# Performance work log

Hardware: AMD Instinct MI355X
Metric: run time of the kernel (lower is better)

## Reference

```python
import jax, jax.numpy as jnp
import numpy as np

B, T, DD, NS, V, E, H, L = 8192, 200, 8, 4, 1000, 32, 256, 2


def setup_inputs() -> dict:
    key = jax.random.key(0)
    ks = jax.random.split(key, 10)
    s = 0.05
    dense = jax.random.normal(ks[0], (B, T, DD), jnp.float32)
    sparse = jax.random.randint(ks[1], (B, T, NS), 0, V)
    lengths = jax.random.randint(ks[2], (B,), 1, T + 1)
    emb_tables = jax.random.normal(ks[3], (NS, V, E), jnp.float32) * s
    Wl = jax.random.normal(ks[4], (H, DD + NS * E), jnp.float32) * s
    bl = jnp.zeros((H,), jnp.float32)
    # axis1: 0 = rnn_entry_exit (even t), 1 = rnn_exit_entry (odd t)
    Wih = jax.random.normal(ks[5], (L, 2, H, H), jnp.float32) * s
    Whh = jax.random.normal(ks[6], (L, 2, H, H), jnp.float32) * s
    bih = jnp.zeros((L, 2, H), jnp.float32)
    bhh = jnp.zeros((L, 2, H), jnp.float32)
    Wout = jax.random.normal(ks[7], (1, H), jnp.float32) * s
    bout = jnp.zeros((1,), jnp.float32)
    return dict(dense=dense, sparse=sparse, lengths=lengths, emb_tables=emb_tables,
                Wl=Wl, bl=bl, Wih=Wih, Whh=Whh, bih=bih, bhh=bhh, Wout=Wout, bout=bout)


def reference(dense, sparse, lengths, emb_tables, Wl, bl, Wih, Whh, bih, bhh, Wout, bout):
    # Padded+mask formulation; equivalent to the packed-sequence loop:
    # finished sequences' hidden states are frozen (== being sliced away),
    # and the final frozen h of the top layer is the per-sequence output.
    # Dropout is identity (eval mode); it is never applied in forward anyway.
    mask = jnp.arange(T)[None, :] < lengths[:, None]        # [B, T]
    d_t = jnp.swapaxes(dense, 0, 1)                          # [T, B, DD]
    s_t = jnp.swapaxes(sparse, 0, 1)                         # [T, B, NS]
    m_t = mask.T                                             # [T, B]

    def embed(st):  # [B, NS] -> [B, NS*E], matching torch.cat of per-feature embeddings
        e = jax.vmap(lambda tab, idx: tab[idx], in_axes=(0, 1), out_axes=1)(emb_tables, st)
        return e.reshape(st.shape[0], NS * E)

    def step(h, xs):  # h: [L, B, H]
        t, dt, st, mt = xs
        x = jnp.concatenate([dt, embed(st)], axis=-1)        # [B, DD+NS*E]
        x = jax.nn.relu(x @ Wl.T + bl)                       # [B, H]
        p = t % 2                                            # which cell set this step
        hs = []
        for i in range(L):
            hn = jnp.tanh(x @ Wih[i, p].T + bih[i, p] + h[i] @ Whh[i, p].T + bhh[i, p])
            hi = jnp.where(mt[:, None], hn, h[i])
            hs.append(hi)
            x = hi
        return jnp.stack(hs), None

    h0 = jnp.zeros((L, B, H), dense.dtype)
    hT, _ = jax.lax.scan(step, h0, (jnp.arange(T), d_t, s_t, m_t))
    return jax.nn.sigmoid(hT[-1] @ Wout.T + bout)[:, 0]     # [B]
```

## Files before the change

### kernel.cpp

```cpp
#include <hip/hip_runtime.h>
#include <math.h>


typedef __attribute__((ext_vector_type(8))) short bf16x8;
typedef __attribute__((ext_vector_type(4))) short s16x4;
typedef __attribute__((ext_vector_type(4))) float f32x4;

#define MFMA(a, b, c) __builtin_amdgcn_mfma_f32_16x16x32_bf16((a), (b), (c), 0, 0, 0)

#define T_  200

#define WLP_OFF   0
#define WIHP_OFF  40960
#define WHHP_OFF  (40960 + 262144)
#define BSUM_BYTE_OFF ((40960 + 262144 + 262144) * 2)

#define XCS 168
#define HS  264
#define SM_XCAT 0
#define SM_XPJ  5376
#define SM_H0   (SM_XPJ + 8448)
#define SM_H1A  (SM_H0 + 8448)
#define SM_H1B  (SM_H1A + 8448)
#define SM_BIAS (SM_H1B + 8448)
#define SM_TOT  (SM_BIAS + 2560)

__device__ __forceinline__ short f2bf(float f) {
    unsigned u = __float_as_uint(f);
    u += 0x7fffu + ((u >> 16) & 1u);
    return (short)(u >> 16);
}
__device__ __forceinline__ float bf2f(short s) {
    return __uint_as_float(((unsigned)(unsigned short)s) << 16);
}
__device__ __forceinline__ float tanh_fast(float x) {
    float e = exp2f(x * 2.88539008f);
    return 1.0f - 2.0f * __builtin_amdgcn_rcpf(e + 1.0f);
}

__global__ void prep_kernel(const float* __restrict__ Wl,
                            const float* __restrict__ Wih,
                            const float* __restrict__ Whh,
                            const float* __restrict__ bih,
                            const float* __restrict__ bhh,
                            short* __restrict__ wsS,
                            float* __restrict__ bsum) {
    int tid = blockIdx.x * 256 + threadIdx.x;
    if (tid < 5120) {
        int mt = tid / 320, rem = tid % 320;
        int kk = rem / 64, lane = rem % 64;
        int o = mt * 16 + (lane & 15);
        int kb = kk * 32 + (lane >> 4) * 8;
        short* dst = wsS + WLP_OFF + tid * 8;
#pragma unroll
        for (int e = 0; e < 8; e++) {
            int k = kb + e;
            dst[e] = f2bf((k < 136) ? Wl[o * 136 + k] : 0.0f);
        }
    } else if (tid < 5120 + 32768) {
        int jj = tid - 5120;
        int mat = jj / 8192, rem = jj % 8192;
        int lane = rem & 63, kk = (rem >> 6) & 7, mt = rem >> 9;
        int o = mt * 16 + (lane & 15);
        int kb = kk * 32 + (lane >> 4) * 8;
        const float* src = Wih + (mat * 256 + o) * 256;
        short* dst = wsS + WIHP_OFF + mat * 65536 + rem * 8;
#pragma unroll
        for (int e = 0; e < 8; e++) dst[e] = f2bf(src[kb + e]);
    } else if (tid < 5120 + 65536) {
        int jj = tid - 37888;
        int mat = jj / 8192, rem = jj % 8192;
        int lane = rem & 63, kk = (rem >> 6) & 7, mt = rem >> 9;
        int o = mt * 16 + (lane & 15);
        int kb = kk * 32 + (lane >> 4) * 8;
        const float* src = Whh + (mat * 256 + o) * 256;
        short* dst = wsS + WHHP_OFF + mat * 65536 + rem * 8;
#pragma unroll
        for (int e = 0; e < 8; e++) dst[e] = f2bf(src[kb + e]);
    } else if (tid < 5120 + 65536 + 1024) {
        int j = tid - 70656;
        bsum[j] = bih[j] + bhh[j];
    }
}

struct GReg { f32x4 e0, e1, dv; };

__device__ __forceinline__ void gather_load(GReg& g, const float* __restrict__ dense,
                                            const int* __restrict__ sparse,
                                            const float* __restrict__ emb,
                                            int b0, int tt, int tid) {
    int gs = tid >> 4, gf = (tid >> 2) & 3, gq = tid & 3;
    int ix = sparse[(b0 + gs) * (T_ * 4) + tt * 4 + gf];
    const float* ep = emb + gf * 32000 + ix * 32 + gq * 8;
    g.e0 = *(const f32x4*)ep;
    g.e1 = *(const f32x4*)(ep + 4);
    if (tid < 64)
        g.dv = *(const f32x4*)(dense + (b0 + (tid >> 1)) * (T_ * 8) + tt * 8 + (tid & 1) * 4);
}
__device__ __forceinline__ void gather_commit(const GReg& g, short* __restrict__ buf, int tid) {
    int gs = tid >> 4, gf = (tid >> 2) & 3, gq = tid & 3;
    s16x4 w0, w1;
#pragma unroll
    for (int r = 0; r < 4; r++) { w0[r] = f2bf(g.e0[r]); w1[r] = f2bf(g.e1[r]); }
    int off = gs * XCS + 8 + gf * 32 + gq * 8;
    *(s16x4*)(buf + off) = w0;
    *(s16x4*)(buf + off + 4) = w1;
    if (tid < 64) {
        s16x4 wd;
#pragma unroll
        for (int r = 0; r < 4; r++) wd[r] = f2bf(g.dv[r]);
        *(s16x4*)(buf + (tid >> 1) * XCS + (tid & 1) * 4) = wd;
    }
}

__device__ __forceinline__ void phaseA(const short* __restrict__ xcat,
                                       short* __restrict__ xpj,
                                       const short* __restrict__ wsS,
                                       const float* __restrict__ blS,
                                       int lane, int lrow, int lgrp, int wid) {
    bf16x8 wl[2][5];
#pragma unroll
    for (int kk = 0; kk < 5; kk++)
#pragma unroll
        for (int mt = 0; mt < 2; mt++)
            wl[mt][kk] = *(const bf16x8*)(wsS + WLP_OFF + (((wid * 2 + mt) * 5 + kk) * 64 + lane) * 8);
    f32x4 xacc[2][2];
#pragma unroll
    for (int mt = 0; mt < 2; mt++) {
        f32x4 bi = *(const f32x4*)(blS + wid * 32 + mt * 16 + lgrp * 4);
        xacc[mt][0] = bi; xacc[mt][1] = bi;
    }
#pragma unroll
    for (int kk = 0; kk < 5; kk++) {
        bf16x8 bxf[2];
#pragma unroll
        for (int nt = 0; nt < 2; nt++)
            bxf[nt] = *(const bf16x8*)(xcat + (nt * 16 + lrow) * XCS + kk * 32 + lgrp * 8);
#pragma unroll
        for (int mt = 0; mt < 2; mt++)
#pragma unroll
            for (int nt = 0; nt < 2; nt++) xacc[mt][nt] = MFMA(wl[mt][kk], bxf[nt], xacc[mt][nt]);
    }
#pragma unroll
    for (int mt = 0; mt < 2; mt++) {
        int o0 = wid * 32 + mt * 16 + lgrp * 4;
#pragma unroll
        for (int nt = 0; nt < 2; nt++) {
            s16x4 w;
#pragma unroll
            for (int r = 0; r < 4; r++) w[r] = f2bf(fmaxf(xacc[mt][nt][r], 0.0f));
            *(s16x4*)(xpj + (nt * 16 + lrow) * HS + o0) = w;
        }
    }
}

__global__ __launch_bounds__(512, 2) void rnn_kernel(
    const float* __restrict__ dense, const int* __restrict__ sparse,
    const int* __restrict__ lengths, const float* __restrict__ emb,
    const float* __restrict__ bl, const float* __restrict__ Wout,
    const float* __restrict__ bout, const short* __restrict__ wsS,
    const float* __restrict__ bsum, float* __restrict__ out) {
    __shared__ alignas(16) short sm[SM_TOT];
    short* xcat = sm + SM_XCAT;
    short* xpj  = sm + SM_XPJ;
    short* h0p  = sm + SM_H0;
    short* h1a  = sm + SM_H1A;
    short* h1b  = sm + SM_H1B;
    float* blS  = (float*)(sm + SM_BIAS);

    const int tid  = threadIdx.x;
    const int wid  = tid >> 6;
    const int lane = tid & 63;
    const int lrow = lane & 15;
    const int lgrp = lane >> 4;
    const int b0   = blockIdx.x * 32;

    for (int i = tid; i < SM_BIAS; i += 512) sm[i] = 0;
    for (int i = tid; i < 1280; i += 512)
        blS[i] = (i < 256) ? bl[i] : bsum[i - 256];

    const int len0 = lengths[b0 + lrow];
    const int len1 = lengths[b0 + 16 + lrow];

    __syncthreads();
    { GReg g0; gather_load(g0, dense, sparse, emb, b0, 0, tid); gather_commit(g0, xcat, tid); }
    __syncthreads();
    phaseA(xcat, xpj, wsS, blS, lane, lrow, lgrp, wid);

    bf16x8 hreg0[2][8];
#pragma unroll
    for (int nt = 0; nt < 2; nt++)
#pragma unroll
        for (int kk = 0; kk < 8; kk++) {
            bf16x8 z;
#pragma unroll
            for (int e = 0; e < 8; e++) z[e] = 0;
            hreg0[nt][kk] = z;
        }
    __syncthreads();

    for (int t = 0; t < T_; t++) {
        const int p = t & 1;
        const bool hasNext = (t + 1 < T_);
        GReg g;
        if (hasNext) gather_load(g, dense, sparse, emb, b0, t + 1, tid);

        {
            const short* Aih = wsS + WIHP_OFF + p * 65536;
            const short* Ahh = wsS + WHHP_OFF + p * 65536;
            bf16x8 wih[2][8], whh[2][8];
#pragma unroll
            for (int kk = 0; kk < 8; kk++)
#pragma unroll
                for (int mt = 0; mt < 2; mt++)
                    wih[mt][kk] = *(const bf16x8*)(Aih + (((wid * 2 + mt) * 8 + kk) * 64 + lane) * 8);
#pragma unroll
            for (int kk = 0; kk < 8; kk++)
#pragma unroll
                for (int mt = 0; mt < 2; mt++)
                    whh[mt][kk] = *(const bf16x8*)(Ahh + (((wid * 2 + mt) * 8 + kk) * 64 + lane) * 8);

            f32x4 acc[2][2];
#pragma unroll
            for (int mt = 0; mt < 2; mt++) {
                f32x4 bi = *(const f32x4*)(blS + 256 + p * 256 + wid * 32 + mt * 16 + lgrp * 4);
                acc[mt][0] = bi; acc[mt][1] = bi;
            }
#pragma unroll
            for (int kk = 0; kk < 8; kk++) {
                bf16x8 bf[2];
#pragma unroll
                for (int nt = 0; nt < 2; nt++)
                    bf[nt] = *(const bf16x8*)(xpj + (nt * 16 + lrow) * HS + kk * 32 + lgrp * 8);
#pragma unroll
                for (int mt = 0; mt < 2; mt++)
#pragma unroll
                    for (int nt = 0; nt < 2; nt++) acc[mt][nt] = MFMA(wih[mt][kk], bf[nt], acc[mt][nt]);
            }
#pragma unroll
            for (int kk = 0; kk < 8; kk++)
#pragma unroll
                for (int mt = 0; mt < 2; mt++)
#pragma unroll
                    for (int nt = 0; nt < 2; nt++) acc[mt][nt] = MFMA(whh[mt][kk], hreg0[nt][kk], acc[mt][nt]);

#pragma unroll
            for (int mt = 0; mt < 2; mt++) {
                int o0 = wid * 32 + mt * 16 + lgrp * 4;
#pragma unroll
                for (int nt = 0; nt < 2; nt++) {
                    s16x4 w;
#pragma unroll
                    for (int r = 0; r < 4; r++) w[r] = f2bf(tanh_fast(acc[mt][nt][r]));
                    int len = nt ? len1 : len0;
                    if (t < len)
                        *(s16x4*)(h0p + (nt * 16 + lrow) * HS + o0) = w;
                }
            }
        }
        if (hasNext) gather_commit(g, xcat, tid);
        __syncthreads();

        {
            const short* h1r = p ? h1b : h1a;
            short* h1w = p ? h1a : h1b;
            const short* Aih = wsS + WIHP_OFF + (2 + p) * 65536;
            const short* Ahh = wsS + WHHP_OFF + (2 + p) * 65536;

#pragma unroll
            for (int nt = 0; nt < 2; nt++)
#pragma unroll
                for (int kk = 0; kk < 8; kk++)
                    hreg0[nt][kk] = *(const bf16x8*)(h0p + (nt * 16 + lrow) * HS + kk * 32 + lgrp * 8);

            bf16x8 wih[2][8], whh[2][8];
#pragma unroll
            for (int kk = 0; kk < 8; kk++)
#pragma unroll
                for (int mt = 0; mt < 2; mt++)
                    wih[mt][kk] = *(const bf16x8*)(Aih + (((wid * 2 + mt) * 8 + kk) * 64 + lane) * 8);
#pragma unroll
            for (int kk = 0; kk < 8; kk++)
#pragma unroll
                for (int mt = 0; mt < 2; mt++)
                    whh[mt][kk] = *(const bf16x8*)(Ahh + (((wid * 2 + mt) * 8 + kk) * 64 + lane) * 8);

            f32x4 acc[2][2];
#pragma unroll
            for (int mt = 0; mt < 2; mt++) {
                f32x4 bi = *(const f32x4*)(blS + 256 + (2 + p) * 256 + wid * 32 + mt * 16 + lgrp * 4);
                acc[mt][0] = bi; acc[mt][1] = bi;
            }
#pragma unroll
            for (int kk = 0; kk < 8; kk++)
#pragma unroll
                for (int mt = 0; mt < 2; mt++)
#pragma unroll
                    for (int nt = 0; nt < 2; nt++) acc[mt][nt] = MFMA(wih[mt][kk], hreg0[nt][kk], acc[mt][nt]);
#pragma unroll
            for (int kk = 0; kk < 8; kk++) {
                bf16x8 bhf[2];
#pragma unroll
                for (int nt = 0; nt < 2; nt++)
                    bhf[nt] = *(const bf16x8*)(h1r + (nt * 16 + lrow) * HS + kk * 32 + lgrp * 8);
#pragma unroll
                for (int mt = 0; mt < 2; mt++)
#pragma unroll
                    for (int nt = 0; nt < 2; nt++) acc[mt][nt] = MFMA(whh[mt][kk], bhf[nt], acc[mt][nt]);
            }

            if (hasNext)
                phaseA(xcat, xpj, wsS, blS, lane, lrow, lgrp, wid);

#pragma unroll
            for (int mt = 0; mt < 2; mt++) {
                int o0 = wid * 32 + mt * 16 + lgrp * 4;
#pragma unroll
                for (int nt = 0; nt < 2; nt++) {
                    int roff = (nt * 16 + lrow) * HS + o0;
                    s16x4 oldv = *(const s16x4*)(h1r + roff);
                    s16x4 w;
#pragma unroll
                    for (int r = 0; r < 4; r++) w[r] = f2bf(tanh_fast(acc[mt][nt][r]));
                    int len = nt ? len1 : len0;
                    *(s16x4*)(h1w + roff) = (t < len) ? w : oldv;
                }
            }
        }
        __syncthreads();
    }

    float* red = (float*)(sm + SM_XPJ);
    if (tid < 256) {
        int s = tid >> 3, part = tid & 7;
        const short* hr = h1a + s * HS + part * 32;
        float sum = 0.0f;
#pragma unroll
        for (int k = 0; k < 32; k++) sum += bf2f(hr[k]) * Wout[part * 32 + k];
        red[s * 8 + part] = sum;
    }
    __syncthreads();
    if (tid < 32) {
        float x = bout[0];
#pragma unroll
        for (int i = 0; i < 8; i++) x += red[tid * 8 + i];
        float e = exp2f(x * 1.44269504f);
        out[b0 + tid] = 1.0f - __builtin_amdgcn_rcpf(1.0f + e);
    }
}

extern "C" void kernel_launch(void* const* d_in, const int* in_sizes, int n_in,
                              void* d_out, int out_size, void* d_ws, size_t ws_size,
                              hipStream_t stream) {
    const float* dense   = (const float*)d_in[0];
    const int*   sparse  = (const int*)d_in[1];
    const int*   lengths = (const int*)d_in[2];
    const float* emb     = (const float*)d_in[3];
    const float* Wl      = (const float*)d_in[4];
    const float* bl      = (const float*)d_in[5];
    const float* Wih     = (const float*)d_in[6];
    const float* Whh     = (const float*)d_in[7];
    const float* bih     = (const float*)d_in[8];
    const float* bhh     = (const float*)d_in[9];
    const float* Wout    = (const float*)d_in[10];
    const float* bout    = (const float*)d_in[11];

    short* wsS  = (short*)d_ws;
    float* bsum = (float*)((char*)d_ws + BSUM_BYTE_OFF);

    prep_kernel<<<280, 256, 0, stream>>>(Wl, Wih, Whh, bih, bhh, wsS, bsum);
    rnn_kernel<<<256, 512, 0, stream>>>(dense, sparse, lengths, emb, bl, Wout, bout,
                                        wsS, bsum, (float*)d_out);
}
```

Measured before the change: 1.421 ms.

## Stream RNN and projection weights through per-wave LDS double-buffered DMA ring

Each wave no longer loads its whole Wih/Whh and Wl fragments into registers. It now prefetches them two k-slices ahead into a per-wave LDS ring using global_load_lds. Ring reads are ordered by explicit vmcnt and lgkmcnt waits, and each layer's input and hidden MFMAs are interleaved per k-slice. The aim is lower register pressure and hiding of the L2 weight-fetch latency behind the MFMA work. The cost is about 64KB of extra LDS, manual waitcnt bookkeeping that also forces the in-flight gather loads to finish early, and a switch of exp2f to the hardware builtin.

```diff
diff --git a/kernel.cpp b/kernel.cpp
--- a/kernel.cpp
+++ b/kernel.cpp
@@ -23,7 +23,8 @@
 #define SM_H1A  (SM_H0 + 8448)
 #define SM_H1B  (SM_H1A + 8448)
 #define SM_BIAS (SM_H1B + 8448)
-#define SM_TOT  (SM_BIAS + 2560)
+#define SM_WRING (SM_BIAS + 2560)
+#define SM_TOT  (SM_WRING + 32768)
 
 __device__ __forceinline__ short f2bf(float f) {
     unsigned u = __float_as_uint(f);
@@ -34,9 +35,23 @@
     return __uint_as_float(((unsigned)(unsigned short)s) << 16);
 }
 __device__ __forceinline__ float tanh_fast(float x) {
-    float e = exp2f(x * 2.88539008f);
+    float e = __builtin_amdgcn_exp2f(x * 2.88539008f);
     return 1.0f - 2.0f * __builtin_amdgcn_rcpf(e + 1.0f);
 }
+
+__device__ __forceinline__ void dma16(const short* g, short* l) {
+    __builtin_amdgcn_global_load_lds(
+        (const __attribute__((address_space(1))) void*)(unsigned long long)(g),
+        (__attribute__((address_space(3))) void*)(unsigned int)(unsigned long long)(l),
+        16, 0, 0);
+}
+
+#define VM_WAIT4() asm volatile("s_waitcnt vmcnt(4)" ::: "memory")
+#define VM_WAIT2() asm volatile("s_waitcnt vmcnt(2)" ::: "memory")
+#define VM_WAIT0() asm volatile("s_waitcnt vmcnt(0)" ::: "memory")
+#define LGKM0()    asm volatile("s_waitcnt lgkmcnt(0)" ::: "memory")
+#define BARRIER()  do { LGKM0(); __builtin_amdgcn_s_barrier(); \
+                        __builtin_amdgcn_sched_barrier(0); } while (0)
 
 __global__ void prep_kernel(const float* __restrict__ Wl,
                             const float* __restrict__ Wih,
@@ -113,17 +128,26 @@
     }
 }
 
-__device__ __forceinline__ void phaseA(const short* __restrict__ xcat,
-                                       short* __restrict__ xpj,
-                                       const short* __restrict__ wsS,
-                                       const float* __restrict__ blS,
-                                       int lane, int lrow, int lgrp, int wid) {
-    bf16x8 wl[2][5];
-#pragma unroll
-    for (int kk = 0; kk < 5; kk++)
-#pragma unroll
-        for (int mt = 0; mt < 2; mt++)
-            wl[mt][kk] = *(const bf16x8*)(wsS + WLP_OFF + (((wid * 2 + mt) * 5 + kk) * 64 + lane) * 8);
+__device__ __forceinline__ void issue4(const short* Aih, const short* Ahh,
+                                       short* slot, int wb, int kk, int lane) {
+#pragma unroll
+    for (int mt = 0; mt < 2; mt++) {
+        dma16(Aih + (((wb + mt) * 8 + kk) * 64 + lane) * 8, slot + mt * 512);
+        dma16(Ahh + (((wb + mt) * 8 + kk) * 64 + lane) * 8, slot + 1024 + mt * 512);
+    }
+}
+__device__ __forceinline__ void issue2(const short* Wlp, short* slot, int wb, int kk, int lane) {
+#pragma unroll
+    for (int mt = 0; mt < 2; mt++)
+        dma16(Wlp + (((wb + mt) * 5 + kk) * 64 + lane) * 8, slot + mt * 512);
+}
+
+__device__ __forceinline__ void phaseA_ring(short* __restrict__ xcat,
+                                            short* __restrict__ xpj,
+                                            const short* __restrict__ Wlp,
+                                            const float* __restrict__ blS,
+                                            short* ring,
+                                            int lane, int lrow, int lgrp, int wid) {
     f32x4 xacc[2][2];
 #pragma unroll
     for (int mt = 0; mt < 2; mt++) {
@@ -132,14 +156,23 @@
     }
 #pragma unroll
     for (int kk = 0; kk < 5; kk++) {
-        bf16x8 bxf[2];
+        short* slot = ring + (kk & 1) * 2048;
+        if (kk == 4) { VM_WAIT0(); } else { VM_WAIT2(); }
+        bf16x8 wl[2], bxf[2];
+#pragma unroll
+        for (int mt = 0; mt < 2; mt++)
+            wl[mt] = *(const bf16x8*)(slot + mt * 512 + lane * 8);
 #pragma unroll
         for (int nt = 0; nt < 2; nt++)
             bxf[nt] = *(const bf16x8*)(xcat + (nt * 16 + lrow) * XCS + kk * 32 + lgrp * 8);
 #pragma unroll
         for (int mt = 0; mt < 2; mt++)
 #pragma unroll
-            for (int nt = 0; nt < 2; nt++) xacc[mt][nt] = MFMA(wl[mt][kk], bxf[nt], xacc[mt][nt]);
+            for (int nt = 0; nt < 2; nt++) xacc[mt][nt] = MFMA(wl[mt], bxf[nt], xacc[mt][nt]);
+        if (kk < 3) {
+            LGKM0();
+            issue2(Wlp, slot, wid * 2, kk + 2, lane);
+        }
     }
 #pragma unroll
     for (int mt = 0; mt < 2; mt++) {
@@ -174,6 +207,8 @@
     const int lrow = lane & 15;
     const int lgrp = lane >> 4;
     const int b0   = blockIdx.x * 32;
+    short* ring = sm + SM_WRING + wid * 4096;
+    const short* Wlp = wsS + WLP_OFF;
 
     for (int i = tid; i < SM_BIAS; i += 512) sm[i] = 0;
     for (int i = tid; i < 1280; i += 512)
@@ -185,7 +220,14 @@
     __syncthreads();
     { GReg g0; gather_load(g0, dense, sparse, emb, b0, 0, tid); gather_commit(g0, xcat, tid); }
     __syncthreads();
-    phaseA(xcat, xpj, wsS, blS, lane, lrow, lgrp, wid);
+
+    issue2(Wlp, ring, wid * 2, 0, lane);
+    issue2(Wlp, ring + 2048, wid * 2, 1, lane);
+    phaseA_ring(xcat, xpj, Wlp, blS, ring, lane, lrow, lgrp, wid);
+    LGKM0();
+    issue4(wsS + WIHP_OFF, wsS + WHHP_OFF, ring,        wid * 2, 0, lane);
+    issue4(wsS + WIHP_OFF, wsS + WHHP_OFF, ring + 2048, wid * 2, 1, lane);
+    BARRIER();
 
     bf16x8 hreg0[2][8];
 #pragma unroll
@@ -197,137 +239,135 @@
             for (int e = 0; e < 8; e++) z[e] = 0;
             hreg0[nt][kk] = z;
         }
-    __syncthreads();
+
+    f32x4 acc[2][2];
 
     for (int t = 0; t < T_; t++) {
         const int p = t & 1;
         const bool hasNext = (t + 1 < T_);
+        const short* Aih1 = wsS + WIHP_OFF + p * 65536;
+        const short* Ahh1 = wsS + WHHP_OFF + p * 65536;
+        const short* Aih2 = wsS + WIHP_OFF + (2 + p) * 65536;
+        const short* Ahh2 = wsS + WHHP_OFF + (2 + p) * 65536;
+
         GReg g;
         if (hasNext) gather_load(g, dense, sparse, emb, b0, t + 1, tid);
 
-        {
-            const short* Aih = wsS + WIHP_OFF + p * 65536;
-            const short* Ahh = wsS + WHHP_OFF + p * 65536;
-            bf16x8 wih[2][8], whh[2][8];
-#pragma unroll
-            for (int kk = 0; kk < 8; kk++)
-#pragma unroll
-                for (int mt = 0; mt < 2; mt++)
-                    wih[mt][kk] = *(const bf16x8*)(Aih + (((wid * 2 + mt) * 8 + kk) * 64 + lane) * 8);
-#pragma unroll
-            for (int kk = 0; kk < 8; kk++)
-#pragma unroll
-                for (int mt = 0; mt < 2; mt++)
-                    whh[mt][kk] = *(const bf16x8*)(Ahh + (((wid * 2 + mt) * 8 + kk) * 64 + lane) * 8);
-
-            f32x4 acc[2][2];
+#pragma unroll
+        for (int mt = 0; mt < 2; mt++) {
+            f32x4 bi = *(const f32x4*)(blS + 256 + p * 256 + wid * 32 + mt * 16 + lgrp * 4);
+            acc[mt][0] = bi; acc[mt][1] = bi;
+        }
+#pragma unroll
+        for (int kk = 0; kk < 8; kk++) {
+            short* slot = ring + (kk & 1) * 2048;
+            if (kk == 7) { VM_WAIT0(); } else { VM_WAIT4(); }
+            bf16x8 aih[2], ahh[2], bxf[2];
 #pragma unroll
             for (int mt = 0; mt < 2; mt++) {
-                f32x4 bi = *(const f32x4*)(blS + 256 + p * 256 + wid * 32 + mt * 16 + lgrp * 4);
-                acc[mt][0] = bi; acc[mt][1] = bi;
-            }
-#pragma unroll
-            for (int kk = 0; kk < 8; kk++) {
-                bf16x8 bf[2];
-#pragma unroll
-                for (int nt = 0; nt < 2; nt++)
-                    bf[nt] = *(const bf16x8*)(xpj + (nt * 16 + lrow) * HS + kk * 32 + lgrp * 8);
-#pragma unroll
-                for (int mt = 0; mt < 2; mt++)
-#pragma unroll
-                    for (int nt = 0; nt < 2; nt++) acc[mt][nt] = MFMA(wih[mt][kk], bf[nt], acc[mt][nt]);
-            }
-#pragma unroll
-            for (int kk = 0; kk < 8; kk++)
-#pragma unroll
-                for (int mt = 0; mt < 2; mt++)
-#pragma unroll
-                    for (int nt = 0; nt < 2; nt++) acc[mt][nt] = MFMA(whh[mt][kk], hreg0[nt][kk], acc[mt][nt]);
-
+                aih[mt] = *(const bf16x8*)(slot + mt * 512 + lane * 8);
+                ahh[mt] = *(const bf16x8*)(slot + 1024 + mt * 512 + lane * 8);
+            }
+#pragma unroll
+            for (int nt = 0; nt < 2; nt++)
+                bxf[nt] = *(const bf16x8*)(xpj + (nt * 16 + lrow) * HS + kk * 32 + lgrp * 8);
+#pragma unroll
+            for (int mt = 0; mt < 2; mt++)
+#pragma unroll
+                for (int nt = 0; nt < 2; nt++) {
+                    acc[mt][nt] = MFMA(aih[mt], bxf[nt], acc[mt][nt]);
+                    acc[mt][nt] = MFMA(ahh[mt], hreg0[nt][kk], acc[mt][nt]);
+                }
+            if (kk < 6) {
+                LGKM0();
+                issue4(Aih1, Ahh1, slot, wid * 2, kk + 2, lane);
+            }
+        }
+#pragma unroll
+        for (int mt = 0; mt < 2; mt++) {
+            int o0 = wid * 32 + mt * 16 + lgrp * 4;
+#pragma unroll
+            for (int nt = 0; nt < 2; nt++) {
+                s16x4 w;
+#pragma unroll
+                for (int r = 0; r < 4; r++) w[r] = f2bf(tanh_fast(acc[mt][nt][r]));
+                int len = nt ? len1 : len0;
+                if (t < len)
+                    *(s16x4*)(h0p + (nt * 16 + lrow) * HS + o0) = w;
+            }
+        }
+        LGKM0();
+        issue4(Aih2, Ahh2, ring,        wid * 2, 0, lane);
+        issue4(Aih2, Ahh2, ring + 2048, wid * 2, 1, lane);
+        if (hasNext) gather_commit(g, xcat, tid);
+        BARRIER();
+
+        const short* h1r = p ? h1b : h1a;
+        short* h1w = p ? h1a : h1b;
+#pragma unroll
+        for (int mt = 0; mt < 2; mt++) {
+            f32x4 bi = *(const f32x4*)(blS + 256 + (2 + p) * 256 + wid * 32 + mt * 16 + lgrp * 4);
+            acc[mt][0] = bi; acc[mt][1] = bi;
+        }
+#pragma unroll
+        for (int kk = 0; kk < 8; kk++) {
+            short* slot = ring + (kk & 1) * 2048;
+            if (kk == 7) { VM_WAIT0(); } else { VM_WAIT4(); }
+            bf16x8 aih[2], ahh[2], bhf[2];
 #pragma unroll
             for (int mt = 0; mt < 2; mt++) {
-                int o0 = wid * 32 + mt * 16 + lgrp * 4;
+                aih[mt] = *(const bf16x8*)(slot + mt * 512 + lane * 8);
+                ahh[mt] = *(const bf16x8*)(slot + 1024 + mt * 512 + lane * 8);
+            }
+#pragma unroll
+            for (int nt = 0; nt < 2; nt++) {
+                hreg0[nt][kk] = *(const bf16x8*)(h0p + (nt * 16 + lrow) * HS + kk * 32 + lgrp * 8);
+                bhf[nt] = *(const bf16x8*)(h1r + (nt * 16 + lrow) * HS + kk * 32 + lgrp * 8);
+            }
+#pragma unroll
+            for (int mt = 0; mt < 2; mt++)
 #pragma unroll
                 for (int nt = 0; nt < 2; nt++) {
-                    s16x4 w;
-#pragma unroll
-                    for (int r = 0; r < 4; r++) w[r] = f2bf(tanh_fast(acc[mt][nt][r]));
-                    int len = nt ? len1 : len0;
-                    if (t < len)
-                        *(s16x4*)(h0p + (nt * 16 + lrow) * HS + o0) = w;
+                    acc[mt][nt] = MFMA(aih[mt], hreg0[nt][kk], acc[mt][nt]);
+                    acc[mt][nt] = MFMA(ahh[mt], bhf[nt], acc[mt][nt]);
                 }
-            }
-        }
-        if (hasNext) gather_commit(g, xcat, tid);
-        __syncthreads();
-
-        {
-            const short* h1r = p ? h1b : h1a;
-            short* h1w = p ? h1a : h1b;
-            const short* Aih = wsS + WIHP_OFF + (2 + p) * 65536;
-            const short* Ahh = wsS + WHHP_OFF + (2 + p) * 65536;
-
-#pragma unroll
-            for (int nt = 0; nt < 2; nt++)
-#pragma unroll
-                for (int kk = 0; kk < 8; kk++)
-                    hreg0[nt][kk] = *(const bf16x8*)(h0p + (nt * 16 + lrow) * HS + kk * 32 + lgrp * 8);
-
-            bf16x8 wih[2][8], whh[2][8];
-#pragma unroll
-            for (int kk = 0; kk < 8; kk++)
-#pragma unroll
-                for (int mt = 0; mt < 2; mt++)
-                    wih[mt][kk] = *(const bf16x8*)(Aih + (((wid * 2 + mt) * 8 + kk) * 64 + lane) * 8);
-#pragma unroll
-            for (int kk = 0; kk < 8; kk++)
-#pragma unroll
-                for (int mt = 0; mt < 2; mt++)
-                    whh[mt][kk] = *(const bf16x8*)(Ahh + (((wid * 2 + mt) * 8 + kk) * 64 + lane) * 8);
-
-            f32x4 acc[2][2];
-#pragma unroll
-            for (int mt = 0; mt < 2; mt++) {
-                f32x4 bi = *(const f32x4*)(blS + 256 + (2 + p) * 256 + wid * 32 + mt * 16 + lgrp * 4);
-                acc[mt][0] = bi; acc[mt][1] = bi;
-            }
-#pragma unroll
-            for (int kk = 0; kk < 8; kk++)
-#pragma unroll
-                for (int mt = 0; mt < 2; mt++)
-#pragma unroll
-                    for (int nt = 0; nt < 2; nt++) acc[mt][nt] = MFMA(wih[mt][kk], hreg0[nt][kk], acc[mt][nt]);
-#pragma unroll
-            for (int kk = 0; kk < 8; kk++) {
-                bf16x8 bhf[2];
-#pragma unroll
-                for (int nt = 0; nt < 2; nt++)
-                    bhf[nt] = *(const bf16x8*)(h1r + (nt * 16 + lrow) * HS + kk * 32 + lgrp * 8);
-#pragma unroll
-                for (int mt = 0; mt < 2; mt++)
-#pragma unroll
-                    for (int nt = 0; nt < 2; nt++) acc[mt][nt] = MFMA(whh[mt][kk], bhf[nt], acc[mt][nt]);
-            }
-
-            if (hasNext)
-                phaseA(xcat, xpj, wsS, blS, lane, lrow, lgrp, wid);
-
-#pragma unroll
-            for (int mt = 0; mt < 2; mt++) {
-                int o0 = wid * 32 + mt * 16 + lgrp * 4;
-#pragma unroll
-                for (int nt = 0; nt < 2; nt++) {
-                    int roff = (nt * 16 + lrow) * HS + o0;
-                    s16x4 oldv = *(const s16x4*)(h1r + roff);
-                    s16x4 w;
-#pragma unroll
-                    for (int r = 0; r < 4; r++) w[r] = f2bf(tanh_fast(acc[mt][nt][r]));
-                    int len = nt ? len1 : len0;
-                    *(s16x4*)(h1w + roff) = (t < len) ? w : oldv;
-                }
-            }
-        }
-        __syncthreads();
+            if (kk < 6) {
+                LGKM0();
+                issue4(Aih2, Ahh2, slot, wid * 2, kk + 2, lane);
+            }
+        }
+
+        if (hasNext) {
+            LGKM0();
+            issue2(Wlp, ring, wid * 2, 0, lane);
+            issue2(Wlp, ring + 2048, wid * 2, 1, lane);
+            phaseA_ring(xcat, xpj, Wlp, blS, ring, lane, lrow, lgrp, wid);
+        }
+
+#pragma unroll
+        for (int mt = 0; mt < 2; mt++) {
+            int o0 = wid * 32 + mt * 16 + lgrp * 4;
+#pragma unroll
+            for (int nt = 0; nt < 2; nt++) {
+                int roff = (nt * 16 + lrow) * HS + o0;
+                s16x4 oldv = *(const s16x4*)(h1r + roff);
+                s16x4 w;
+#pragma unroll
+                for (int r = 0; r < 4; r++) w[r] = f2bf(tanh_fast(acc[mt][nt][r]));
+                int len = nt ? len1 : len0;
+                *(s16x4*)(h1w + roff) = (t < len) ? w : oldv;
+            }
+        }
+
+        if (hasNext) {
+            LGKM0();
+            int pn = p ^ 1;
+            issue4(wsS + WIHP_OFF + pn * 65536, wsS + WHHP_OFF + pn * 65536,
+                   ring,        wid * 2, 0, lane);
+            issue4(wsS + WIHP_OFF + pn * 65536, wsS + WHHP_OFF + pn * 65536,
+                   ring + 2048, wid * 2, 1, lane);
+        }
+        BARRIER();
     }
 
     float* red = (float*)(sm + SM_XPJ);
@@ -344,7 +384,7 @@
         float x = bout[0];
 #pragma unroll
         for (int i = 0; i < 8; i++) x += red[tid * 8 + i];
-        float e = exp2f(x * 1.44269504f);
+        float e = __builtin_amdgcn_exp2f(x * 1.44269504f);
         out[b0 + tid] = 1.0f - __builtin_amdgcn_rcpf(1.0f + e);
     }
 }
```

Result: faster. 1.375 ms (-3.2%).

## Stream recurrent weights through a 3-deep register ring instead of preloading all

Applied to the files above, without the earlier changes.

The recurrent and projection weight fragments are no longer loaded in full (32 bf16x8 registers per layer) before the MFMAs start. They now go through a triple-buffered register ring that prefetches two k-slices ahead, and the ih and hh MFMAs are interleaved within each k step. This cuts register pressure and lets global/L2 weight loads overlap with compute. Launch bounds drop to one block per SM-equivalent, and exp2f is replaced by the hardware exp2 builtin. The lower occupancy hint may reduce latency hiding, and smaller prefetch depth could expose load latency.

```diff
diff --git a/kernel.cpp b/kernel.cpp
--- a/kernel.cpp
+++ b/kernel.cpp
@@ -34,7 +34,7 @@
     return __uint_as_float(((unsigned)(unsigned short)s) << 16);
 }
 __device__ __forceinline__ float tanh_fast(float x) {
-    float e = exp2f(x * 2.88539008f);
+    float e = __builtin_amdgcn_exp2f(x * 2.88539008f);
     return 1.0f - 2.0f * __builtin_amdgcn_rcpf(e + 1.0f);
 }
 
@@ -115,15 +115,15 @@
 
 __device__ __forceinline__ void phaseA(const short* __restrict__ xcat,
                                        short* __restrict__ xpj,
-                                       const short* __restrict__ wsS,
+                                       const short* __restrict__ Wlp,
                                        const float* __restrict__ blS,
                                        int lane, int lrow, int lgrp, int wid) {
-    bf16x8 wl[2][5];
-#pragma unroll
-    for (int kk = 0; kk < 5; kk++)
-#pragma unroll
-        for (int mt = 0; mt < 2; mt++)
-            wl[mt][kk] = *(const bf16x8*)(wsS + WLP_OFF + (((wid * 2 + mt) * 5 + kk) * 64 + lane) * 8);
+    bf16x8 wl[3][2];
+#pragma unroll
+    for (int j = 0; j < 2; j++) {
+        wl[j][0] = *(const bf16x8*)(Wlp + (((wid * 2 + 0) * 5 + j) * 64 + lane) * 8);
+        wl[j][1] = *(const bf16x8*)(Wlp + (((wid * 2 + 1) * 5 + j) * 64 + lane) * 8);
+    }
     f32x4 xacc[2][2];
 #pragma unroll
     for (int mt = 0; mt < 2; mt++) {
@@ -132,6 +132,12 @@
     }
 #pragma unroll
     for (int kk = 0; kk < 5; kk++) {
+        const int cur = kk % 3;
+        if (kk < 3) {
+            const int nxt = (kk + 2) % 3;
+            wl[nxt][0] = *(const bf16x8*)(Wlp + (((wid * 2 + 0) * 5 + kk + 2) * 64 + lane) * 8);
+            wl[nxt][1] = *(const bf16x8*)(Wlp + (((wid * 2 + 1) * 5 + kk + 2) * 64 + lane) * 8);
+        }
         bf16x8 bxf[2];
 #pragma unroll
         for (int nt = 0; nt < 2; nt++)
@@ -139,7 +145,7 @@
 #pragma unroll
         for (int mt = 0; mt < 2; mt++)
 #pragma unroll
-            for (int nt = 0; nt < 2; nt++) xacc[mt][nt] = MFMA(wl[mt][kk], bxf[nt], xacc[mt][nt]);
+            for (int nt = 0; nt < 2; nt++) xacc[mt][nt] = MFMA(wl[cur][mt], bxf[nt], xacc[mt][nt]);
     }
 #pragma unroll
     for (int mt = 0; mt < 2; mt++) {
@@ -154,7 +160,7 @@
     }
 }
 
-__global__ __launch_bounds__(512, 2) void rnn_kernel(
+__global__ __launch_bounds__(512, 1) void rnn_kernel(
     const float* __restrict__ dense, const int* __restrict__ sparse,
     const int* __restrict__ lengths, const float* __restrict__ emb,
     const float* __restrict__ bl, const float* __restrict__ Wout,
@@ -174,6 +180,7 @@
     const int lrow = lane & 15;
     const int lgrp = lane >> 4;
     const int b0   = blockIdx.x * 32;
+    const short* Wlp = wsS + WLP_OFF;
 
     for (int i = tid; i < SM_BIAS; i += 512) sm[i] = 0;
     for (int i = tid; i < 1280; i += 512)
@@ -185,7 +192,7 @@
     __syncthreads();
     { GReg g0; gather_load(g0, dense, sparse, emb, b0, 0, tid); gather_commit(g0, xcat, tid); }
     __syncthreads();
-    phaseA(xcat, xpj, wsS, blS, lane, lrow, lgrp, wid);
+    phaseA(xcat, xpj, Wlp, blS, lane, lrow, lgrp, wid);
 
     bf16x8 hreg0[2][8];
 #pragma unroll
@@ -202,24 +209,23 @@
     for (int t = 0; t < T_; t++) {
         const int p = t & 1;
         const bool hasNext = (t + 1 < T_);
+        const short* Aih1 = wsS + WIHP_OFF + p * 65536;
+        const short* Ahh1 = wsS + WHHP_OFF + p * 65536;
+        const short* Aih2 = wsS + WIHP_OFF + (2 + p) * 65536;
+        const short* Ahh2 = wsS + WHHP_OFF + (2 + p) * 65536;
+
         GReg g;
         if (hasNext) gather_load(g, dense, sparse, emb, b0, t + 1, tid);
 
         {
-            const short* Aih = wsS + WIHP_OFF + p * 65536;
-            const short* Ahh = wsS + WHHP_OFF + p * 65536;
-            bf16x8 wih[2][8], whh[2][8];
-#pragma unroll
-            for (int kk = 0; kk < 8; kk++)
-#pragma unroll
-                for (int mt = 0; mt < 2; mt++)
-                    wih[mt][kk] = *(const bf16x8*)(Aih + (((wid * 2 + mt) * 8 + kk) * 64 + lane) * 8);
-#pragma unroll
-            for (int kk = 0; kk < 8; kk++)
-#pragma unroll
-                for (int mt = 0; mt < 2; mt++)
-                    whh[mt][kk] = *(const bf16x8*)(Ahh + (((wid * 2 + mt) * 8 + kk) * 64 + lane) * 8);
-
+            bf16x8 wa[3][4];
+#pragma unroll
+            for (int j = 0; j < 2; j++) {
+                wa[j][0] = *(const bf16x8*)(Aih1 + (((wid * 2 + 0) * 8 + j) * 64 + lane) * 8);
+                wa[j][1] = *(const bf16x8*)(Aih1 + (((wid * 2 + 1) * 8 + j) * 64 + lane) * 8);
+                wa[j][2] = *(const bf16x8*)(Ahh1 + (((wid * 2 + 0) * 8 + j) * 64 + lane) * 8);
+                wa[j][3] = *(const bf16x8*)(Ahh1 + (((wid * 2 + 1) * 8 + j) * 64 + lane) * 8);
+            }
             f32x4 acc[2][2];
 #pragma unroll
             for (int mt = 0; mt < 2; mt++) {
@@ -228,22 +234,26 @@
             }
 #pragma unroll
             for (int kk = 0; kk < 8; kk++) {
-                bf16x8 bf[2];
+                const int cur = kk % 3;
+                if (kk < 6) {
+                    const int nxt = (kk + 2) % 3;
+                    wa[nxt][0] = *(const bf16x8*)(Aih1 + (((wid * 2 + 0) * 8 + kk + 2) * 64 + lane) * 8);
+                    wa[nxt][1] = *(const bf16x8*)(Aih1 + (((wid * 2 + 1) * 8 + kk + 2) * 64 + lane) * 8);
+                    wa[nxt][2] = *(const bf16x8*)(Ahh1 + (((wid * 2 + 0) * 8 + kk + 2) * 64 + lane) * 8);
+                    wa[nxt][3] = *(const bf16x8*)(Ahh1 + (((wid * 2 + 1) * 8 + kk + 2) * 64 + lane) * 8);
+                }
+                bf16x8 bxf[2];
 #pragma unroll
                 for (int nt = 0; nt < 2; nt++)
-                    bf[nt] = *(const bf16x8*)(xpj + (nt * 16 + lrow) * HS + kk * 32 + lgrp * 8);
+                    bxf[nt] = *(const bf16x8*)(xpj + (nt * 16 + lrow) * HS + kk * 32 + lgrp * 8);
 #pragma unroll
                 for (int mt = 0; mt < 2; mt++)
 #pragma unroll
-                    for (int nt = 0; nt < 2; nt++) acc[mt][nt] = MFMA(wih[mt][kk], bf[nt], acc[mt][nt]);
-            }
-#pragma unroll
-            for (int kk = 0; kk < 8; kk++)
-#pragma unroll
-                for (int mt = 0; mt < 2; mt++)
-#pragma unroll
-                    for (int nt = 0; nt < 2; nt++) acc[mt][nt] = MFMA(whh[mt][kk], hreg0[nt][kk], acc[mt][nt]);
-
+                    for (int nt = 0; nt < 2; nt++) {
+                        acc[mt][nt] = MFMA(wa[cur][mt], bxf[nt], acc[mt][nt]);
+                        acc[mt][nt] = MFMA(wa[cur][2 + mt], hreg0[nt][kk], acc[mt][nt]);
+                    }
+            }
 #pragma unroll
             for (int mt = 0; mt < 2; mt++) {
                 int o0 = wid * 32 + mt * 16 + lgrp * 4;
@@ -264,27 +274,15 @@
         {
             const short* h1r = p ? h1b : h1a;
             short* h1w = p ? h1a : h1b;
-            const short* Aih = wsS + WIHP_OFF + (2 + p) * 65536;
-            const short* Ahh = wsS + WHHP_OFF + (2 + p) * 65536;
-
-#pragma unroll
-            for (int nt = 0; nt < 2; nt++)
-#pragma unroll
-                for (int kk = 0; kk < 8; kk++)
-                    hreg0[nt][kk] = *(const bf16x8*)(h0p + (nt * 16 + lrow) * HS + kk * 32 + lgrp * 8);
-
-            bf16x8 wih[2][8], whh[2][8];
-#pragma unroll
-            for (int kk = 0; kk < 8; kk++)
-#pragma unroll
-                for (int mt = 0; mt < 2; mt++)
-                    wih[mt][kk] = *(const bf16x8*)(Aih + (((wid * 2 + mt) * 8 + kk) * 64 + lane) * 8);
-#pragma unroll
-            for (int kk = 0; kk < 8; kk++)
-#pragma unroll
-                for (int mt = 0; mt < 2; mt++)
-                    whh[mt][kk] = *(const bf16x8*)(Ahh + (((wid * 2 + mt) * 8 + kk) * 64 + lane) * 8);
-
+
+            bf16x8 wa[3][4];
+#pragma unroll
+            for (int j = 0; j < 2; j++) {
+                wa[j][0] = *(const bf16x8*)(Aih2 + (((wid * 2 + 0) * 8 + j) * 64 + lane) * 8);
+                wa[j][1] = *(const bf16x8*)(Aih2 + (((wid * 2 + 1) * 8 + j) * 64 + lane) * 8);
+                wa[j][2] = *(const bf16x8*)(Ahh2 + (((wid * 2 + 0) * 8 + j) * 64 + lane) * 8);
+                wa[j][3] = *(const bf16x8*)(Ahh2 + (((wid * 2 + 1) * 8 + j) * 64 + lane) * 8);
+            }
             f32x4 acc[2][2];
 #pragma unroll
             for (int mt = 0; mt < 2; mt++) {
@@ -292,25 +290,32 @@
                 acc[mt][0] = bi; acc[mt][1] = bi;
             }
 #pragma unroll
-            for (int kk = 0; kk < 8; kk++)
+            for (int kk = 0; kk < 8; kk++) {
+                const int cur = kk % 3;
+                if (kk < 6) {
+                    const int nxt = (kk + 2) % 3;
+                    wa[nxt][0] = *(const bf16x8*)(Aih2 + (((wid * 2 + 0) * 8 + kk + 2) * 64 + lane) * 8);
+                    wa[nxt][1] = *(const bf16x8*)(Aih2 + (((wid * 2 + 1) * 8 + kk + 2) * 64 + lane) * 8);
+                    wa[nxt][2] = *(const bf16x8*)(Ahh2 + (((wid * 2 + 0) * 8 + kk + 2) * 64 + lane) * 8);
+                    wa[nxt][3] = *(const bf16x8*)(Ahh2 + (((wid * 2 + 1) * 8 + kk + 2) * 64 + lane) * 8);
+                }
+                bf16x8 bhf[2];
+#pragma unroll
+                for (int nt = 0; nt < 2; nt++) {
+                    hreg0[nt][kk] = *(const bf16x8*)(h0p + (nt * 16 + lrow) * HS + kk * 32 + lgrp * 8);
+                    bhf[nt] = *(const bf16x8*)(h1r + (nt * 16 + lrow) * HS + kk * 32 + lgrp * 8);
+                }
 #pragma unroll
                 for (int mt = 0; mt < 2; mt++)
 #pragma unroll
-                    for (int nt = 0; nt < 2; nt++) acc[mt][nt] = MFMA(wih[mt][kk], hreg0[nt][kk], acc[mt][nt]);
-#pragma unroll
-            for (int kk = 0; kk < 8; kk++) {
-                bf16x8 bhf[2];
-#pragma unroll
-                for (int nt = 0; nt < 2; nt++)
-                    bhf[nt] = *(const bf16x8*)(h1r + (nt * 16 + lrow) * HS + kk * 32 + lgrp * 8);
-#pragma unroll
-                for (int mt = 0; mt < 2; mt++)
-#pragma unroll
-                    for (int nt = 0; nt < 2; nt++) acc[mt][nt] = MFMA(whh[mt][kk], bhf[nt], acc[mt][nt]);
+                    for (int nt = 0; nt < 2; nt++) {
+                        acc[mt][nt] = MFMA(wa[cur][mt], hreg0[nt][kk], acc[mt][nt]);
+                        acc[mt][nt] = MFMA(wa[cur][2 + mt], bhf[nt], acc[mt][nt]);
+                    }
             }
 
             if (hasNext)
-                phaseA(xcat, xpj, wsS, blS, lane, lrow, lgrp, wid);
+                phaseA(xcat, xpj, Wlp, blS, lane, lrow, lgrp, wid);
 
 #pragma unroll
             for (int mt = 0; mt < 2; mt++) {
@@ -344,7 +349,7 @@
         float x = bout[0];
 #pragma unroll
         for (int i = 0; i < 8; i++) x += red[tid * 8 + i];
-        float e = exp2f(x * 1.44269504f);
+        float e = __builtin_amdgcn_exp2f(x * 1.44269504f);
         out[b0 + tid] = 1.0f - __builtin_amdgcn_rcpf(1.0f + e);
     }
 }
```

After: 1.205 ms. 15.2% less time.
